# Kernel tuning notes

Measured on AMD Instinct MI355X. Metric: run time of the kernel, lower is better.

The kernel has to match this reference:

```python
import jax, jax.numpy as jnp
import numpy as np

N_NODES = 50000
N_EDGES = 1600000
N_HEAD = 4
F_OUT = 128


def setup_inputs() -> dict:
    key = jax.random.key(0)
    k1, k2, k3, k4 = jax.random.split(key, 4)
    x = jax.random.normal(k1, (N_NODES, F_OUT), dtype=jnp.float32)
    # diag weight [H,1,F]; small scale like xavier on a diag-ish param
    w = jax.random.normal(k2, (N_HEAD, 1, F_OUT), dtype=jnp.float32) * 0.1
    # a_src_dst init: uniform(-stdv, stdv), stdv = 1/sqrt(2*f_out)
    stdv = 1.0 / np.sqrt(2 * F_OUT)
    a = jax.random.uniform(k3, (N_HEAD, 2 * F_OUT, 1), dtype=jnp.float32, minval=-stdv, maxval=stdv)
    edge_index = jax.random.randint(k4, (2, N_EDGES), 0, N_NODES, dtype=jnp.int64)
    return {"x": x, "w": w, "a": a, "edge_index": edge_index}


def reference(x, w, a, edge_index):
    # x: [N,F], w: [H,1,F] (diag), a: [H,2F,1], edge_index: [2,E]
    H, F = w.shape[0], w.shape[-1]
    N = x.shape[0]
    src = edge_index[0]  # row indices (aggregation targets)
    dst = edge_index[1]
    h = x[None, :, :] * w  # [H,N,F]  (diag: elementwise scale per head)
    # split cat(h_src,h_dst)@a into two per-node projections (same math as concat+matmul)
    a_src = a[:, :F, 0]  # [H,F]
    a_dst = a[:, F:, 0]  # [H,F]
    s_src = jnp.einsum('hnf,hf->hn', h, a_src)  # [H,N]
    s_dst = jnp.einsum('hnf,hf->hn', h, a_dst)  # [H,N]
    score = s_src[:, src] + s_dst[:, dst]  # [H,E]
    edge_e = jnp.exp(-jax.nn.leaky_relu(score, negative_slope=0.2))  # [H,E]
    outs = []
    for i in range(H):  # small fixed head loop keeps peak memory at one head's messages
        rowsum = jax.ops.segment_sum(edge_e[i], src, num_segments=N)  # [N]
        msg = edge_e[i][:, None] * h[i][dst]  # [E,F]
        agg = jax.ops.segment_sum(msg, src, num_segments=N)  # [N,F]
        outs.append(agg / rowsum[:, None])
    return jnp.stack(outs, axis=0)  # [H,N,F]
```

## Files before the change

kernel.cpp:

```cpp
#include <hip/hip_runtime.h>

#define N_NODES 50000
#define N_EDGES 1600000
#define N_HEAD 4
#define F_OUT 128
#define CAP 96
#define NPS 512
#define K1 98
#define SCAP 17408
#define NPG 64
#define GROUPS 782
#define EPB 2048
#define P1_BLOCKS ((N_EDGES + EPB - 1) / EPB)
#define SCORE_BLOCKS ((N_NODES * 64 + 255) / 256)
#define FUSED_BLOCKS (P1_BLOCKS + SCORE_BLOCKS)

__global__ void __launch_bounds__(256) prep_kernel(
    const float* __restrict__ x, const float* __restrict__ w,
    const float* __restrict__ a, float4* __restrict__ s_src4,
    float4* __restrict__ s_dst4,
    const int* __restrict__ src, const int* __restrict__ dst,
    int* __restrict__ gc, unsigned int* __restrict__ region) {
  __shared__ int hist[K1], cur[K1], lstart[K1], gpos[K1];
  __shared__ unsigned int staging[EPB];
  const int tid = threadIdx.x;

  if (blockIdx.x >= P1_BLOCKS) {
    int bid = blockIdx.x - P1_BLOCKS;
    int wv = (bid * 256 + tid) >> 6;
    int lane = tid & 63;
    if (wv >= N_NODES) return;
    float xv0 = x[wv * F_OUT + lane];
    float xv1 = x[wv * F_OUT + 64 + lane];
    float ps[N_HEAD], pd[N_HEAD];
#pragma unroll
    for (int h = 0; h < N_HEAD; ++h) {
      float w0 = w[h * F_OUT + lane];
      float w1 = w[h * F_OUT + 64 + lane];
      float as0 = a[h * 2 * F_OUT + lane];
      float as1 = a[h * 2 * F_OUT + 64 + lane];
      float ad0 = a[h * 2 * F_OUT + F_OUT + lane];
      float ad1 = a[h * 2 * F_OUT + F_OUT + 64 + lane];
      ps[h] = xv0 * w0 * as0 + xv1 * w1 * as1;
      pd[h] = xv0 * w0 * ad0 + xv1 * w1 * ad1;
    }
#pragma unroll
    for (int off = 32; off > 0; off >>= 1) {
#pragma unroll
      for (int h = 0; h < N_HEAD; ++h) {
        ps[h] += __shfl_xor(ps[h], off, 64);
        pd[h] += __shfl_xor(pd[h], off, 64);
      }
    }
    if (lane == 0) {
      s_src4[wv] = make_float4(ps[0], ps[1], ps[2], ps[3]);
      s_dst4[wv] = make_float4(pd[0], pd[1], pd[2], pd[3]);
    }
    return;
  }

  const int base = blockIdx.x * EPB;
  int vc = N_EDGES - base;
  if (vc > EPB) vc = EPB;

  unsigned int pk[EPB / 256];
#pragma unroll
  for (int k = 0; k < EPB / 256; ++k) {
    int i = k * 256 + tid;
    if (i < vc) {
      unsigned int s = (unsigned int)src[base + i];
      unsigned int d = (unsigned int)dst[base + i];
      pk[k] = (s << 16) | d;
    } else {
      pk[k] = 0xffffffffu;
    }
  }
  if (tid < K1) { hist[tid] = 0; cur[tid] = 0; }
  __syncthreads();
#pragma unroll
  for (int k = 0; k < EPB / 256; ++k)
    if (pk[k] != 0xffffffffu) atomicAdd(&hist[pk[k] >> 25], 1);
  __syncthreads();
  if (tid < 64) {
    int carry = 0;
    for (int b0 = 0; b0 < K1; b0 += 64) {
      int idx = b0 + tid;
      int h = (idx < K1) ? hist[idx] : 0;
      int v = h;
#pragma unroll
      for (int off = 1; off < 64; off <<= 1) {
        int t = __shfl_up(v, off, 64);
        if (tid >= off) v += t;
      }
      if (idx < K1) {
        lstart[idx] = carry + v - h;
        gpos[idx] = atomicAdd(&gc[idx], h);
      }
      carry += __shfl(v, 63, 64);
    }
  }
  __syncthreads();
#pragma unroll
  for (int k = 0; k < EPB / 256; ++k) {
    if (pk[k] != 0xffffffffu) {
      int b = pk[k] >> 25;
      int pos = lstart[b] + atomicAdd(&cur[b], 1);
      staging[pos] = pk[k];
    }
  }
  __syncthreads();
  for (int i = tid; i < vc; i += 256) {
    unsigned int v = staging[i];
    int b = v >> 25;
    int off = gpos[b] + (i - lstart[b]);
    if (off < SCAP) region[(size_t)b * SCAP + off] = v;
  }
}


#define EDGE_FMA(W, X)                                                     \
  acc0.x = fmaf(W.x, X.x, acc0.x); acc0.y = fmaf(W.x, X.y, acc0.y);        \
  acc0.z = fmaf(W.x, X.z, acc0.z); acc0.w = fmaf(W.x, X.w, acc0.w);        \
  acc1.x = fmaf(W.y, X.x, acc1.x); acc1.y = fmaf(W.y, X.y, acc1.y);        \
  acc1.z = fmaf(W.y, X.z, acc1.z); acc1.w = fmaf(W.y, X.w, acc1.w);        \
  acc2.x = fmaf(W.z, X.x, acc2.x); acc2.y = fmaf(W.z, X.y, acc2.y);        \
  acc2.z = fmaf(W.z, X.z, acc2.z); acc2.w = fmaf(W.z, X.w, acc2.w);        \
  acc3.x = fmaf(W.w, X.x, acc3.x); acc3.y = fmaf(W.w, X.y, acc3.y);        \
  acc3.z = fmaf(W.w, X.z, acc3.z); acc3.w = fmaf(W.w, X.w, acc3.w);

#define SCAN_PROC(v)                                                       \
  {                                                                        \
    unsigned int s_ = (v) >> 16;                                           \
    if ((s_ >> 6) == gtag) {                                               \
      int l_ = s_ & 63;                                                    \
      int p_ = atomicAdd(&ncnt[l_], 1);                                    \
      if (p_ < CAP) nbkt[l_][p_] = (int)((v) & 0xffffu);                   \
    }                                                                      \
  }

__global__ void __launch_bounds__(512, 6) agg_kernel(
    const float* __restrict__ x, const float* __restrict__ w,
    const float4* __restrict__ s_src4, const float4* __restrict__ s_dst4,
    const int* __restrict__ gc, const unsigned int* __restrict__ region,
    float* __restrict__ out) {
  __shared__ int ncnt[NPG];
  __shared__ int nbkt[NPG][CAP];
  __shared__ float4 lds_w[8][CAP];
  const int tid = threadIdx.x;
  const int g = blockIdx.x;
  const int sb = g >> 3;
  int c = gc[sb];
  if (c > SCAP) c = SCAP;
  if (tid < NPG) ncnt[tid] = 0;
  __syncthreads();

  const unsigned int* reg = region + (size_t)sb * SCAP;
  const unsigned int gtag = (unsigned int)g;
  {
    int i = tid;
    for (; i + 1536 < c; i += 2048) {
      unsigned int v0 = reg[i];
      unsigned int v1 = reg[i + 512];
      unsigned int v2 = reg[i + 1024];
      unsigned int v3 = reg[i + 1536];
      SCAN_PROC(v0); SCAN_PROC(v1); SCAN_PROC(v2); SCAN_PROC(v3);
    }
    for (; i < c; i += 512) { unsigned int v0 = reg[i]; SCAN_PROC(v0); }
  }
  __syncthreads();

  const int ws = tid >> 6, lane = tid & 63;
  const int half = lane >> 5;
  const int sl = lane & 31;
  const float4* x4 = (const float4*)x;

  for (int l = ws; l < NPG; l += 8) {
    int n = g * NPG + l;
    if (n >= N_NODES) break;
    int m = ncnt[l];
    m = (m < CAP) ? m : CAP;
    float4 ss = s_src4[n];

    float p0 = 0.f, p1 = 0.f, p2 = 0.f, p3 = 0.f;
    for (int j = lane; j < m; j += 64) {
      int d = nbkt[l][j];
      float4 sd = s_dst4[d];
      float sc0 = ss.x + sd.x, sc1 = ss.y + sd.y, sc2 = ss.z + sd.z, sc3 = ss.w + sd.w;
      float e0 = __expf(-fmaxf(sc0, 0.2f * sc0));
      float e1 = __expf(-fmaxf(sc1, 0.2f * sc1));
      float e2 = __expf(-fmaxf(sc2, 0.2f * sc2));
      float e3 = __expf(-fmaxf(sc3, 0.2f * sc3));
      lds_w[ws][j] = make_float4(e0, e1, e2, e3);
      p0 += e0; p1 += e1; p2 += e2; p3 += e3;
    }
    int m_pad = (m + 7) & ~7;
    if (lane < m_pad - m) {
      nbkt[l][m + lane] = 0;
      lds_w[ws][m + lane] = make_float4(0.f, 0.f, 0.f, 0.f);
    }

    float4 acc0 = {0.f, 0.f, 0.f, 0.f}, acc1 = {0.f, 0.f, 0.f, 0.f};
    float4 acc2 = {0.f, 0.f, 0.f, 0.f}, acc3 = {0.f, 0.f, 0.f, 0.f};
    for (int t = 0; t < m_pad; t += 8) {
      int e0 = t + half, e1 = t + 2 + half, e2 = t + 4 + half, e3 = t + 6 + half;
      int d0 = nbkt[l][e0];
      int d1 = nbkt[l][e1];
      int d2 = nbkt[l][e2];
      int d3 = nbkt[l][e3];
      float4 x0 = x4[(size_t)d0 * 32 + sl];
      float4 x1 = x4[(size_t)d1 * 32 + sl];
      float4 x2 = x4[(size_t)d2 * 32 + sl];
      float4 x3 = x4[(size_t)d3 * 32 + sl];
      float4 w0 = lds_w[ws][e0];
      float4 w1 = lds_w[ws][e1];
      float4 w2 = lds_w[ws][e2];
      float4 w3 = lds_w[ws][e3];
      EDGE_FMA(w0, x0)
      EDGE_FMA(w1, x1)
      EDGE_FMA(w2, x2)
      EDGE_FMA(w3, x3)
    }

    acc0.x += __shfl_xor(acc0.x, 32, 64); acc0.y += __shfl_xor(acc0.y, 32, 64);
    acc0.z += __shfl_xor(acc0.z, 32, 64); acc0.w += __shfl_xor(acc0.w, 32, 64);
    acc1.x += __shfl_xor(acc1.x, 32, 64); acc1.y += __shfl_xor(acc1.y, 32, 64);
    acc1.z += __shfl_xor(acc1.z, 32, 64); acc1.w += __shfl_xor(acc1.w, 32, 64);
    acc2.x += __shfl_xor(acc2.x, 32, 64); acc2.y += __shfl_xor(acc2.y, 32, 64);
    acc2.z += __shfl_xor(acc2.z, 32, 64); acc2.w += __shfl_xor(acc2.w, 32, 64);
    acc3.x += __shfl_xor(acc3.x, 32, 64); acc3.y += __shfl_xor(acc3.y, 32, 64);
    acc3.z += __shfl_xor(acc3.z, 32, 64); acc3.w += __shfl_xor(acc3.w, 32, 64);

#pragma unroll
    for (int off = 32; off > 0; off >>= 1) {
      p0 += __shfl_xor(p0, off, 64);
      p1 += __shfl_xor(p1, off, 64);
      p2 += __shfl_xor(p2, off, 64);
      p3 += __shfl_xor(p3, off, 64);
    }
    float r0 = 1.f / p0, r1 = 1.f / p1, r2 = 1.f / p2, r3 = 1.f / p3;

    const float4* w4 = (const float4*)w;
    float4 wA = w4[(half ? 1 : 0) * 32 + sl];
    float4 wB = w4[(half ? 3 : 2) * 32 + sl];
    float4 aA = half ? acc1 : acc0;
    float4 aB = half ? acc3 : acc2;
    float rA = half ? r1 : r0;
    float rB = half ? r3 : r2;
    float4 o;
    o.x = wA.x * aA.x * rA; o.y = wA.y * aA.y * rA;
    o.z = wA.z * aA.z * rA; o.w = wA.w * aA.w * rA;
    *(float4*)(out + ((size_t)half * N_NODES + n) * F_OUT + 4 * sl) = o;
    o.x = wB.x * aB.x * rB; o.y = wB.y * aB.y * rB;
    o.z = wB.z * aB.z * rB; o.w = wB.w * aB.w * rB;
    *(float4*)(out + ((size_t)(2 + half) * N_NODES + n) * F_OUT + 4 * sl) = o;
  }
}

extern "C" void kernel_launch(void* const* d_in, const int* in_sizes, int n_in,
                              void* d_out, int out_size, void* d_ws, size_t ws_size,
                              hipStream_t stream) {
  const float* x = (const float*)d_in[0];
  const float* w = (const float*)d_in[1];
  const float* a = (const float*)d_in[2];
  const int* ei = (const int*)d_in[3];
  const int* src = ei;
  const int* dst = ei + N_EDGES;
  float* out = (float*)d_out;

  char* p = (char*)d_ws;
  float4* s_src4 = (float4*)p;      p += (size_t)N_NODES * 16;
  float4* s_dst4 = (float4*)p;      p += (size_t)N_NODES * 16;
  int* gc = (int*)p;                p += 4096;
  unsigned int* region = (unsigned int*)p;
  p += (size_t)K1 * SCAP * 4;

  hipMemsetAsync(gc, 0, 4096, stream);

  prep_kernel<<<FUSED_BLOCKS, 256, 0, stream>>>(x, w, a, s_src4, s_dst4,
                                                src, dst, gc, region);
  agg_kernel<<<GROUPS, 512, 0, stream>>>(x, w, s_src4, s_dst4, gc, region, out);
}
```

Before: 310.5 us.

## Fuse edge-weight computation into gather loop and halve nodes per block

Edge attention weights are now computed inline in the gather loop rather than in a separate pass staged through shared memory. Padding slots point to a sentinel node whose s_dst is infinity, so their exp weight is zero. Blocks now cover 32 nodes with 256 threads, the bucket scan reads uint4, and s_src for the next node is prefetched. The exps are computed redundantly by the 32 lanes of each half-wave, and each block rescans its shared region with twice as many blocks doing so.

```diff
diff --git a/kernel.cpp b/kernel.cpp
--- a/kernel.cpp
+++ b/kernel.cpp
@@ -8,8 +8,8 @@
 #define NPS 512
 #define K1 98
 #define SCAP 17408
-#define NPG 64
-#define GROUPS 782
+#define NPG 32
+#define GROUPS 1563
 #define EPB 2048
 #define P1_BLOCKS ((N_EDGES + EPB - 1) / EPB)
 #define SCORE_BLOCKS ((N_NODES * 64 + 255) / 256)
@@ -27,6 +27,9 @@
 
   if (blockIdx.x >= P1_BLOCKS) {
     int bid = blockIdx.x - P1_BLOCKS;
+    if (bid == 0 && tid == 0) {
+      s_dst4[N_NODES] = make_float4(INFINITY, INFINITY, INFINITY, INFINITY);
+    }
     int wv = (bid * 256 + tid) >> 6;
     int lane = tid & 63;
     if (wv >= N_NODES) return;
@@ -118,37 +121,26 @@
 }
 
 
-#define EDGE_FMA(W, X)                                                     \
-  acc0.x = fmaf(W.x, X.x, acc0.x); acc0.y = fmaf(W.x, X.y, acc0.y);        \
-  acc0.z = fmaf(W.x, X.z, acc0.z); acc0.w = fmaf(W.x, X.w, acc0.w);        \
-  acc1.x = fmaf(W.y, X.x, acc1.x); acc1.y = fmaf(W.y, X.y, acc1.y);        \
-  acc1.z = fmaf(W.y, X.z, acc1.z); acc1.w = fmaf(W.y, X.w, acc1.w);        \
-  acc2.x = fmaf(W.z, X.x, acc2.x); acc2.y = fmaf(W.z, X.y, acc2.y);        \
-  acc2.z = fmaf(W.z, X.z, acc2.z); acc2.w = fmaf(W.z, X.w, acc2.w);        \
-  acc3.x = fmaf(W.w, X.x, acc3.x); acc3.y = fmaf(W.w, X.y, acc3.y);        \
-  acc3.z = fmaf(W.w, X.z, acc3.z); acc3.w = fmaf(W.w, X.w, acc3.w);
-
 #define SCAN_PROC(v)                                                       \
   {                                                                        \
     unsigned int s_ = (v) >> 16;                                           \
-    if ((s_ >> 6) == gtag) {                                               \
-      int l_ = s_ & 63;                                                    \
+    if ((s_ >> 5) == gtag) {                                               \
+      int l_ = s_ & 31;                                                    \
       int p_ = atomicAdd(&ncnt[l_], 1);                                    \
       if (p_ < CAP) nbkt[l_][p_] = (int)((v) & 0xffffu);                   \
     }                                                                      \
   }
 
-__global__ void __launch_bounds__(512, 6) agg_kernel(
+__global__ void __launch_bounds__(256, 6) agg_kernel(
     const float* __restrict__ x, const float* __restrict__ w,
     const float4* __restrict__ s_src4, const float4* __restrict__ s_dst4,
     const int* __restrict__ gc, const unsigned int* __restrict__ region,
     float* __restrict__ out) {
   __shared__ int ncnt[NPG];
   __shared__ int nbkt[NPG][CAP];
-  __shared__ float4 lds_w[8][CAP];
   const int tid = threadIdx.x;
   const int g = blockIdx.x;
-  const int sb = g >> 3;
+  const int sb = g >> 4;
   int c = gc[sb];
   if (c > SCAP) c = SCAP;
   if (tid < NPG) ncnt[tid] = 0;
@@ -157,15 +149,16 @@
   const unsigned int* reg = region + (size_t)sb * SCAP;
   const unsigned int gtag = (unsigned int)g;
   {
-    int i = tid;
-    for (; i + 1536 < c; i += 2048) {
-      unsigned int v0 = reg[i];
-      unsigned int v1 = reg[i + 512];
-      unsigned int v2 = reg[i + 1024];
-      unsigned int v3 = reg[i + 1536];
-      SCAN_PROC(v0); SCAN_PROC(v1); SCAN_PROC(v2); SCAN_PROC(v3);
-    }
-    for (; i < c; i += 512) { unsigned int v0 = reg[i]; SCAN_PROC(v0); }
+    const uint4* reg4 = (const uint4*)reg;
+    int c4 = c >> 2;
+    for (int i = tid; i < c4; i += 256) {
+      uint4 v = reg4[i];
+      SCAN_PROC(v.x); SCAN_PROC(v.y); SCAN_PROC(v.z); SCAN_PROC(v.w);
+    }
+    for (int i = (c4 << 2) + tid; i < c; i += 256) {
+      unsigned int v = reg[i];
+      SCAN_PROC(v);
+    }
   }
   __syncthreads();
 
@@ -174,52 +167,64 @@
   const int sl = lane & 31;
   const float4* x4 = (const float4*)x;
 
-  for (int l = ws; l < NPG; l += 8) {
+  const float4* w4 = (const float4*)w;
+  const float4 wA = w4[(half ? 1 : 0) * 32 + sl];
+  const float4 wB = w4[(half ? 3 : 2) * 32 + sl];
+
+  float4 ss = s_src4[g * NPG + ws];
+
+  for (int l = ws; l < NPG; l += 4) {
     int n = g * NPG + l;
     if (n >= N_NODES) break;
+    int nn = n + 4;
+    if (nn > N_NODES - 1) nn = N_NODES - 1;
+    float4 ss_next = s_src4[nn];
+
     int m = ncnt[l];
     m = (m < CAP) ? m : CAP;
-    float4 ss = s_src4[n];
-
-    float p0 = 0.f, p1 = 0.f, p2 = 0.f, p3 = 0.f;
-    for (int j = lane; j < m; j += 64) {
-      int d = nbkt[l][j];
-      float4 sd = s_dst4[d];
-      float sc0 = ss.x + sd.x, sc1 = ss.y + sd.y, sc2 = ss.z + sd.z, sc3 = ss.w + sd.w;
-      float e0 = __expf(-fmaxf(sc0, 0.2f * sc0));
-      float e1 = __expf(-fmaxf(sc1, 0.2f * sc1));
-      float e2 = __expf(-fmaxf(sc2, 0.2f * sc2));
-      float e3 = __expf(-fmaxf(sc3, 0.2f * sc3));
-      lds_w[ws][j] = make_float4(e0, e1, e2, e3);
-      p0 += e0; p1 += e1; p2 += e2; p3 += e3;
-    }
     int m_pad = (m + 7) & ~7;
-    if (lane < m_pad - m) {
-      nbkt[l][m + lane] = 0;
-      lds_w[ws][m + lane] = make_float4(0.f, 0.f, 0.f, 0.f);
-    }
+    if (lane < m_pad - m) nbkt[l][m + lane] = N_NODES;
 
     float4 acc0 = {0.f, 0.f, 0.f, 0.f}, acc1 = {0.f, 0.f, 0.f, 0.f};
     float4 acc2 = {0.f, 0.f, 0.f, 0.f}, acc3 = {0.f, 0.f, 0.f, 0.f};
+    float p0 = 0.f, p1 = 0.f, p2 = 0.f, p3 = 0.f;
+
     for (int t = 0; t < m_pad; t += 8) {
-      int e0 = t + half, e1 = t + 2 + half, e2 = t + 4 + half, e3 = t + 6 + half;
-      int d0 = nbkt[l][e0];
-      int d1 = nbkt[l][e1];
-      int d2 = nbkt[l][e2];
-      int d3 = nbkt[l][e3];
-      float4 x0 = x4[(size_t)d0 * 32 + sl];
-      float4 x1 = x4[(size_t)d1 * 32 + sl];
-      float4 x2 = x4[(size_t)d2 * 32 + sl];
-      float4 x3 = x4[(size_t)d3 * 32 + sl];
-      float4 w0 = lds_w[ws][e0];
-      float4 w1 = lds_w[ws][e1];
-      float4 w2 = lds_w[ws][e2];
-      float4 w3 = lds_w[ws][e3];
-      EDGE_FMA(w0, x0)
-      EDGE_FMA(w1, x1)
-      EDGE_FMA(w2, x2)
-      EDGE_FMA(w3, x3)
-    }
+      int dd[4];
+      float4 sd[4], xv[4];
+#pragma unroll
+      for (int q = 0; q < 4; ++q) dd[q] = nbkt[l][t + 2 * q + half];
+#pragma unroll
+      for (int q = 0; q < 4; ++q) sd[q] = s_dst4[dd[q]];
+#pragma unroll
+      for (int q = 0; q < 4; ++q) {
+        int dx = dd[q] < N_NODES - 1 ? dd[q] : N_NODES - 1;
+        xv[q] = x4[(size_t)dx * 32 + sl];
+      }
+#pragma unroll
+      for (int q = 0; q < 4; ++q) {
+        float s0 = ss.x + sd[q].x, s1 = ss.y + sd[q].y;
+        float s2 = ss.z + sd[q].z, s3 = ss.w + sd[q].w;
+        float e0 = __expf(-fmaxf(s0, 0.2f * s0));
+        float e1 = __expf(-fmaxf(s1, 0.2f * s1));
+        float e2 = __expf(-fmaxf(s2, 0.2f * s2));
+        float e3 = __expf(-fmaxf(s3, 0.2f * s3));
+        p0 += e0; p1 += e1; p2 += e2; p3 += e3;
+        acc0.x = fmaf(e0, xv[q].x, acc0.x); acc0.y = fmaf(e0, xv[q].y, acc0.y);
+        acc0.z = fmaf(e0, xv[q].z, acc0.z); acc0.w = fmaf(e0, xv[q].w, acc0.w);
+        acc1.x = fmaf(e1, xv[q].x, acc1.x); acc1.y = fmaf(e1, xv[q].y, acc1.y);
+        acc1.z = fmaf(e1, xv[q].z, acc1.z); acc1.w = fmaf(e1, xv[q].w, acc1.w);
+        acc2.x = fmaf(e2, xv[q].x, acc2.x); acc2.y = fmaf(e2, xv[q].y, acc2.y);
+        acc2.z = fmaf(e2, xv[q].z, acc2.z); acc2.w = fmaf(e2, xv[q].w, acc2.w);
+        acc3.x = fmaf(e3, xv[q].x, acc3.x); acc3.y = fmaf(e3, xv[q].y, acc3.y);
+        acc3.z = fmaf(e3, xv[q].z, acc3.z); acc3.w = fmaf(e3, xv[q].w, acc3.w);
+      }
+    }
+
+    p0 += __shfl_xor(p0, 32, 64);
+    p1 += __shfl_xor(p1, 32, 64);
+    p2 += __shfl_xor(p2, 32, 64);
+    p3 += __shfl_xor(p3, 32, 64);
 
     acc0.x += __shfl_xor(acc0.x, 32, 64); acc0.y += __shfl_xor(acc0.y, 32, 64);
     acc0.z += __shfl_xor(acc0.z, 32, 64); acc0.w += __shfl_xor(acc0.w, 32, 64);
@@ -230,18 +235,8 @@
     acc3.x += __shfl_xor(acc3.x, 32, 64); acc3.y += __shfl_xor(acc3.y, 32, 64);
     acc3.z += __shfl_xor(acc3.z, 32, 64); acc3.w += __shfl_xor(acc3.w, 32, 64);
 
-#pragma unroll
-    for (int off = 32; off > 0; off >>= 1) {
-      p0 += __shfl_xor(p0, off, 64);
-      p1 += __shfl_xor(p1, off, 64);
-      p2 += __shfl_xor(p2, off, 64);
-      p3 += __shfl_xor(p3, off, 64);
-    }
     float r0 = 1.f / p0, r1 = 1.f / p1, r2 = 1.f / p2, r3 = 1.f / p3;
 
-    const float4* w4 = (const float4*)w;
-    float4 wA = w4[(half ? 1 : 0) * 32 + sl];
-    float4 wB = w4[(half ? 3 : 2) * 32 + sl];
     float4 aA = half ? acc1 : acc0;
     float4 aB = half ? acc3 : acc2;
     float rA = half ? r1 : r0;
@@ -253,6 +248,8 @@
     o.x = wB.x * aB.x * rB; o.y = wB.y * aB.y * rB;
     o.z = wB.z * aB.z * rB; o.w = wB.w * aB.w * rB;
     *(float4*)(out + ((size_t)(2 + half) * N_NODES + n) * F_OUT + 4 * sl) = o;
+
+    ss = ss_next;
   }
 }
 
@@ -268,8 +265,8 @@
   float* out = (float*)d_out;
 
   char* p = (char*)d_ws;
-  float4* s_src4 = (float4*)p;      p += (size_t)N_NODES * 16;
-  float4* s_dst4 = (float4*)p;      p += (size_t)N_NODES * 16;
+  float4* s_src4 = (float4*)p;      p += (size_t)(N_NODES + 1) * 16;
+  float4* s_dst4 = (float4*)p;      p += (size_t)(N_NODES + 1) * 16;
   int* gc = (int*)p;                p += 4096;
   unsigned int* region = (unsigned int*)p;
   p += (size_t)K1 * SCAP * 4;
@@ -278,5 +275,5 @@
 
   prep_kernel<<<FUSED_BLOCKS, 256, 0, stream>>>(x, w, a, s_src4, s_dst4,
                                                 src, dst, gc, region);
-  agg_kernel<<<GROUPS, 512, 0, stream>>>(x, w, s_src4, s_dst4, gc, region, out);
+  agg_kernel<<<GROUPS, 256, 0, stream>>>(x, w, s_src4, s_dst4, gc, region, out);
 }
```

After: 335.7 us. 8.1% more time.

## Halve nodes per aggregation block and deepen gather unroll with vectorized region scan

Applied to the files above, without the earlier changes.

Cuts nodes per block from 64 to 32 and threads from 512 to 256, doubling the block count, so each block scans its super-bucket region twice as often. The region scan now reads uint4 vectors, and the gather loop handles 16 edges per iteration so more independent x loads are in flight. The w loads move out of the per-node loop. The trade is more redundant region scanning across blocks and higher register pressure from the deeper unroll, against better memory-level parallelism and finer load balance.

```diff
diff --git a/kernel.cpp b/kernel.cpp
--- a/kernel.cpp
+++ b/kernel.cpp
@@ -8,8 +8,8 @@
 #define NPS 512
 #define K1 98
 #define SCAP 17408
-#define NPG 64
-#define GROUPS 782
+#define NPG 32
+#define GROUPS 1563
 #define EPB 2048
 #define P1_BLOCKS ((N_EDGES + EPB - 1) / EPB)
 #define SCORE_BLOCKS ((N_NODES * 64 + 255) / 256)
@@ -131,24 +131,24 @@
 #define SCAN_PROC(v)                                                       \
   {                                                                        \
     unsigned int s_ = (v) >> 16;                                           \
-    if ((s_ >> 6) == gtag) {                                               \
-      int l_ = s_ & 63;                                                    \
+    if ((s_ >> 5) == gtag) {                                               \
+      int l_ = s_ & 31;                                                    \
       int p_ = atomicAdd(&ncnt[l_], 1);                                    \
       if (p_ < CAP) nbkt[l_][p_] = (int)((v) & 0xffffu);                   \
     }                                                                      \
   }
 
-__global__ void __launch_bounds__(512, 6) agg_kernel(
+__global__ void __launch_bounds__(256, 4) agg_kernel(
     const float* __restrict__ x, const float* __restrict__ w,
     const float4* __restrict__ s_src4, const float4* __restrict__ s_dst4,
     const int* __restrict__ gc, const unsigned int* __restrict__ region,
     float* __restrict__ out) {
   __shared__ int ncnt[NPG];
   __shared__ int nbkt[NPG][CAP];
-  __shared__ float4 lds_w[8][CAP];
+  __shared__ float4 lds_w[4][CAP];
   const int tid = threadIdx.x;
   const int g = blockIdx.x;
-  const int sb = g >> 3;
+  const int sb = g >> 4;
   int c = gc[sb];
   if (c > SCAP) c = SCAP;
   if (tid < NPG) ncnt[tid] = 0;
@@ -157,15 +157,16 @@
   const unsigned int* reg = region + (size_t)sb * SCAP;
   const unsigned int gtag = (unsigned int)g;
   {
-    int i = tid;
-    for (; i + 1536 < c; i += 2048) {
-      unsigned int v0 = reg[i];
-      unsigned int v1 = reg[i + 512];
-      unsigned int v2 = reg[i + 1024];
-      unsigned int v3 = reg[i + 1536];
-      SCAN_PROC(v0); SCAN_PROC(v1); SCAN_PROC(v2); SCAN_PROC(v3);
-    }
-    for (; i < c; i += 512) { unsigned int v0 = reg[i]; SCAN_PROC(v0); }
+    const uint4* reg4 = (const uint4*)reg;
+    int c4 = c >> 2;
+    for (int i = tid; i < c4; i += 256) {
+      uint4 v = reg4[i];
+      SCAN_PROC(v.x); SCAN_PROC(v.y); SCAN_PROC(v.z); SCAN_PROC(v.w);
+    }
+    for (int i = (c4 << 2) + tid; i < c; i += 256) {
+      unsigned int v = reg[i];
+      SCAN_PROC(v);
+    }
   }
   __syncthreads();
 
@@ -174,7 +175,11 @@
   const int sl = lane & 31;
   const float4* x4 = (const float4*)x;
 
-  for (int l = ws; l < NPG; l += 8) {
+  const float4* w4 = (const float4*)w;
+  const float4 wA = w4[(half ? 1 : 0) * 32 + sl];
+  const float4 wB = w4[(half ? 3 : 2) * 32 + sl];
+
+  for (int l = ws; l < NPG; l += 4) {
     int n = g * NPG + l;
     if (n >= N_NODES) break;
     int m = ncnt[l];
@@ -193,7 +198,7 @@
       lds_w[ws][j] = make_float4(e0, e1, e2, e3);
       p0 += e0; p1 += e1; p2 += e2; p3 += e3;
     }
-    int m_pad = (m + 7) & ~7;
+    int m_pad = (m + 15) & ~15;
     if (lane < m_pad - m) {
       nbkt[l][m + lane] = 0;
       lds_w[ws][m + lane] = make_float4(0.f, 0.f, 0.f, 0.f);
@@ -201,24 +206,17 @@
 
     float4 acc0 = {0.f, 0.f, 0.f, 0.f}, acc1 = {0.f, 0.f, 0.f, 0.f};
     float4 acc2 = {0.f, 0.f, 0.f, 0.f}, acc3 = {0.f, 0.f, 0.f, 0.f};
-    for (int t = 0; t < m_pad; t += 8) {
-      int e0 = t + half, e1 = t + 2 + half, e2 = t + 4 + half, e3 = t + 6 + half;
-      int d0 = nbkt[l][e0];
-      int d1 = nbkt[l][e1];
-      int d2 = nbkt[l][e2];
-      int d3 = nbkt[l][e3];
-      float4 x0 = x4[(size_t)d0 * 32 + sl];
-      float4 x1 = x4[(size_t)d1 * 32 + sl];
-      float4 x2 = x4[(size_t)d2 * 32 + sl];
-      float4 x3 = x4[(size_t)d3 * 32 + sl];
-      float4 w0 = lds_w[ws][e0];
-      float4 w1 = lds_w[ws][e1];
-      float4 w2 = lds_w[ws][e2];
-      float4 w3 = lds_w[ws][e3];
-      EDGE_FMA(w0, x0)
-      EDGE_FMA(w1, x1)
-      EDGE_FMA(w2, x2)
-      EDGE_FMA(w3, x3)
+    for (int t = 0; t < m_pad; t += 16) {
+      int dd[8];
+      float4 xv[8], wv[8];
+#pragma unroll
+      for (int q = 0; q < 8; ++q) dd[q] = nbkt[l][t + 2 * q + half];
+#pragma unroll
+      for (int q = 0; q < 8; ++q) xv[q] = x4[(size_t)dd[q] * 32 + sl];
+#pragma unroll
+      for (int q = 0; q < 8; ++q) wv[q] = lds_w[ws][t + 2 * q + half];
+#pragma unroll
+      for (int q = 0; q < 8; ++q) { EDGE_FMA(wv[q], xv[q]) }
     }
 
     acc0.x += __shfl_xor(acc0.x, 32, 64); acc0.y += __shfl_xor(acc0.y, 32, 64);
@@ -239,9 +237,6 @@
     }
     float r0 = 1.f / p0, r1 = 1.f / p1, r2 = 1.f / p2, r3 = 1.f / p3;
 
-    const float4* w4 = (const float4*)w;
-    float4 wA = w4[(half ? 1 : 0) * 32 + sl];
-    float4 wB = w4[(half ? 3 : 2) * 32 + sl];
     float4 aA = half ? acc1 : acc0;
     float4 aB = half ? acc3 : acc2;
     float rA = half ? r1 : r0;
@@ -268,8 +263,8 @@
   float* out = (float*)d_out;
 
   char* p = (char*)d_ws;
-  float4* s_src4 = (float4*)p;      p += (size_t)N_NODES * 16;
-  float4* s_dst4 = (float4*)p;      p += (size_t)N_NODES * 16;
+  float4* s_src4 = (float4*)p;      p += (size_t)(N_NODES + 1) * 16;
+  float4* s_dst4 = (float4*)p;      p += (size_t)(N_NODES + 1) * 16;
   int* gc = (int*)p;                p += 4096;
   unsigned int* region = (unsigned int*)p;
   p += (size_t)K1 * SCAP * 4;
@@ -278,5 +273,5 @@
 
   prep_kernel<<<FUSED_BLOCKS, 256, 0, stream>>>(x, w, a, s_src4, s_dst4,
                                                 src, dst, gc, region);
-  agg_kernel<<<GROUPS, 512, 0, stream>>>(x, w, s_src4, s_dst4, gc, region, out);
+  agg_kernel<<<GROUPS, 256, 0, stream>>>(x, w, s_src4, s_dst4, gc, region, out);
 }
```

Result: faster. 296.8 us (-4.4%).
